# Optimization experiments

Hardware: AMD Instinct MI355X
Metric: run time of the kernel (lower is better)

Reference implementation:

```python
import jax, jax.numpy as jnp
import numpy as np

DIM = 1024
N_HEADS = 16
HEAD_DIM = DIM // N_HEADS
LN_EPS = 1e-5


def layer_norm(x, gamma, beta):
    mu = jnp.mean(x, axis=-1, keepdims=True)
    var = jnp.var(x, axis=-1, keepdims=True)
    return (x - mu) * jax.lax.rsqrt(var + LN_EPS) * gamma + beta


def setup_inputs() -> dict:
    key = jax.random.key(0)
    ks = jax.random.split(key, 12)
    B, Nq, Nc, D = 2, 2048, 2048, DIM
    s = 1.0 / np.sqrt(D)
    return {
        "query": jax.random.normal(ks[0], (B, Nq, D), jnp.float32),
        "context": jax.random.normal(ks[1], (B, Nc, D), jnp.float32),
        "Wq": jax.random.normal(ks[2], (D, D), jnp.float32) * s,
        "bq": jnp.zeros((D,), jnp.float32),
        "Wk": jax.random.normal(ks[3], (D, D), jnp.float32) * s,
        "bk": jnp.zeros((D,), jnp.float32),
        "Wv": jax.random.normal(ks[4], (D, D), jnp.float32) * s,
        "bv": jnp.zeros((D,), jnp.float32),
        "Wo": jax.random.normal(ks[5], (D, D), jnp.float32) * s,
        "bo": jnp.zeros((D,), jnp.float32),
        "gq": jnp.ones((D,), jnp.float32),
        "betaq": jnp.zeros((D,), jnp.float32),
        "gkv": jnp.ones((D,), jnp.float32),
        "betakv": jnp.zeros((D,), jnp.float32),
    }


def reference(query, context, Wq, bq, Wk, bk, Wv, bv, Wo, bo, gq, betaq, gkv, betakv):
    B, Nq, D = query.shape
    Nc = context.shape[1]
    residual = query
    q = layer_norm(query, gq, betaq)
    c = layer_norm(context, gkv, betakv)
    # projections; (B,N,D) -> (B,H,N,hd)
    Q = (q @ Wq + bq).reshape(B, Nq, N_HEADS, HEAD_DIM).transpose(0, 2, 1, 3)
    K = (c @ Wk + bk).reshape(B, Nc, N_HEADS, HEAD_DIM).transpose(0, 2, 1, 3)
    V = (c @ Wv + bv).reshape(B, Nc, N_HEADS, HEAD_DIM).transpose(0, 2, 1, 3)
    scores = jnp.einsum("bhqd,bhkd->bhqk", Q, K) / np.sqrt(HEAD_DIM).astype(np.float32)
    attn = jax.nn.softmax(scores, axis=-1)
    out = jnp.einsum("bhqk,bhkd->bhqd", attn, V)
    out = out.transpose(0, 2, 1, 3).reshape(B, Nq, D)
    return residual + out @ Wo + bo
```

## Files before the change

### kernel.cpp

```cpp
#include <hip/hip_runtime.h>
#include <hip/hip_bf16.h>

typedef unsigned short u16;
typedef unsigned long long u64;
typedef __bf16 bf16x8 __attribute__((ext_vector_type(8)));
typedef float f32x4 __attribute__((ext_vector_type(4)));

#define DIM 1024
#define NH 16
#define HD 64
#define QSCALE 0.180336880972788f

__device__ __forceinline__ u16 f2bf(float f) {
  union { float f; unsigned u; } v; v.f = f;
  unsigned r = v.u + 0x7fffu + ((v.u >> 16) & 1u);
  return (u16)(r >> 16);
}

__device__ __forceinline__ unsigned pk2(float a, float b) {
  union { __hip_bfloat162 h; unsigned u; } cv;
  cv.h = __float22bfloat162_rn(make_float2(a, b));
  return cv.u;
}

__device__ __forceinline__ float bf2f(unsigned s) {
  union { unsigned u; float f; } v; v.u = s << 16; return v.f;
}

__device__ __forceinline__ float fexp2(float x) {
#if __has_builtin(__builtin_amdgcn_exp2f)
  return __builtin_amdgcn_exp2f(x);
#else
  return exp2f(x);
#endif
}

__device__ __forceinline__ void gld16(const u16* gp, u16* lp) {
  __builtin_amdgcn_global_load_lds(
      (const __attribute__((address_space(1))) unsigned int*)(const void*)gp,
      (__attribute__((address_space(3))) unsigned int*)(void*)lp, 16, 0, 0);
}

__global__ __launch_bounds__(256) void prep_kernel(
    const float* __restrict__ q, const float* __restrict__ c,
    const float* __restrict__ gq, const float* __restrict__ bq,
    const float* __restrict__ gkv, const float* __restrict__ bkv,
    u16* __restrict__ qn, u16* __restrict__ cn,
    const float* W0, const float* W1, const float* W2, const float* W3,
    u16* O0, u16* O1, u16* O2, u16* O3) {
  __shared__ float red[2][4];
  __shared__ float t[32][33];
  int bid = blockIdx.x, tid = threadIdx.x;
  if (bid < 8192) {
    const float* x  = bid < 4096 ? q : c;
    const float* g  = bid < 4096 ? gq : gkv;
    const float* be = bid < 4096 ? bq : bkv;
    u16* out = bid < 4096 ? qn : cn;
    int row = bid & 4095;
    float4 v = ((const float4*)(x + (size_t)row * DIM))[tid];
    float s1 = v.x + v.y + v.z + v.w;
    float s2 = v.x * v.x + v.y * v.y + v.z * v.z + v.w * v.w;
#pragma unroll
    for (int o = 32; o >= 1; o >>= 1) { s1 += __shfl_xor(s1, o, 64); s2 += __shfl_xor(s2, o, 64); }
    int wv = tid >> 6;
    if ((tid & 63) == 0) { red[0][wv] = s1; red[1][wv] = s2; }
    __syncthreads();
    s1 = red[0][0] + red[0][1] + red[0][2] + red[0][3];
    s2 = red[1][0] + red[1][1] + red[1][2] + red[1][3];
    float mu = s1 * (1.f / DIM);
    float var = s2 * (1.f / DIM) - mu * mu;
    float rs = rsqrtf(var + 1e-5f);
    float4 gv = ((const float4*)g)[tid];
    float4 bv = ((const float4*)be)[tid];
    uint2 o2;
    o2.x = pk2((v.x - mu) * rs * gv.x + bv.x, (v.y - mu) * rs * gv.y + bv.y);
    o2.y = pk2((v.z - mu) * rs * gv.z + bv.z, (v.w - mu) * rs * gv.w + bv.w);
    ((uint2*)(out + (size_t)row * DIM))[tid] = o2;
  } else {
    int wid = bid - 8192;
    int z = wid >> 10;
    const float* W = z == 0 ? W0 : z == 1 ? W1 : z == 2 ? W2 : W3;
    u16* O        = z == 0 ? O0 : z == 1 ? O1 : z == 2 ? O2 : O3;
    int xy = wid & 1023;
    int bx = (xy & 31) * 32, by = (xy >> 5) * 32;
    int tx = tid & 31, ty = tid >> 5;
#pragma unroll
    for (int i = 0; i < 4; ++i) t[ty + i * 8][tx] = W[(size_t)(by + ty + i * 8) * DIM + bx + tx];
    __syncthreads();
#pragma unroll
    for (int i = 0; i < 4; ++i) O[(size_t)(bx + ty + i * 8) * DIM + by + tx] = f2bf(t[tx][ty + i * 8]);
  }
}

__global__ __launch_bounds__(256) void gemm_qkv(
    const u16* __restrict__ qn, const u16* __restrict__ cn,
    const u16* __restrict__ Wqt, const u16* __restrict__ Wkt, const u16* __restrict__ Wvt,
    const float* __restrict__ bq, const float* __restrict__ bk, const float* __restrict__ bv,
    u16* __restrict__ Qb, u16* __restrict__ Kb, u16* __restrict__ Vtb) {
  __shared__ __align__(16) u16 sm[(128 + 64 + 64) * 64];
  u16* As  = sm;
  u16* B0s = sm + 128 * 64;
  u16* B1s = sm + 192 * 64;
  int tid = threadIdx.x, wave = tid >> 6, lane = tid & 63;
  int lr = lane & 15, quad = lane >> 4;
  int m0 = blockIdx.x * 128, n0 = blockIdx.y * 64;
  int wm = (wave >> 1) * 64, wn = (wave & 1) * 32;

  if (blockIdx.z == 0) {
    f32x4 acck[4][2] = {}, accv[4][2] = {};
    for (int kt = 0; kt < DIM; kt += 64) {
#pragma unroll
      for (int r = 0; r < 4; ++r) {
        int slot = tid + r * 256;
        int row = slot >> 3;
        int c = (slot & 7) ^ (row & 7);
        gld16(cn + (size_t)(m0 + row) * DIM + kt + c * 8, &As[slot * 8]);
      }
      {
        int slot = tid;
        int row = slot >> 3;
        int c = (slot & 7) ^ (row & 7);
        gld16(Wkt + (size_t)(n0 + row) * DIM + kt + c * 8, &B0s[slot * 8]);
        gld16(Wvt + (size_t)(n0 + row) * DIM + kt + c * 8, &B1s[slot * 8]);
        slot = tid + 256; row = slot >> 3; c = (slot & 7) ^ (row & 7);
        gld16(Wkt + (size_t)(n0 + row) * DIM + kt + c * 8, &B0s[slot * 8]);
        gld16(Wvt + (size_t)(n0 + row) * DIM + kt + c * 8, &B1s[slot * 8]);
      }
      __syncthreads();
#pragma unroll
      for (int kc = 0; kc < 2; ++kc) {
        int pc = ((kc * 4 + quad) ^ (lr & 7)) * 8;
        bf16x8 af[4], b0f[2], b1f[2];
#pragma unroll
        for (int i = 0; i < 4; ++i) af[i] = *(const bf16x8*)&As[(wm + i * 16 + lr) * 64 + pc];
#pragma unroll
        for (int j = 0; j < 2; ++j) {
          b0f[j] = *(const bf16x8*)&B0s[(wn + j * 16 + lr) * 64 + pc];
          b1f[j] = *(const bf16x8*)&B1s[(wn + j * 16 + lr) * 64 + pc];
        }
#pragma unroll
        for (int mi = 0; mi < 4; ++mi)
#pragma unroll
          for (int ni = 0; ni < 2; ++ni) {
            acck[mi][ni] = __builtin_amdgcn_mfma_f32_16x16x32_bf16(af[mi], b0f[ni], acck[mi][ni], 0, 0, 0);
            accv[mi][ni] = __builtin_amdgcn_mfma_f32_16x16x32_bf16(b1f[ni], af[mi], accv[mi][ni], 0, 0, 0);
          }
      }
      __syncthreads();
    }
#pragma unroll
    for (int mi = 0; mi < 4; ++mi)
#pragma unroll
      for (int ni = 0; ni < 2; ++ni) {
        int col = n0 + wn + ni * 16 + lr;
        float bb_ = bk[col];
        int row0 = m0 + wm + mi * 16 + quad * 4;
#pragma unroll
        for (int r = 0; r < 4; ++r)
          Kb[(size_t)(row0 + r) * DIM + col] = f2bf(acck[mi][ni][r] + bb_);
      }
#pragma unroll
    for (int mi = 0; mi < 4; ++mi) {
      int m = m0 + wm + mi * 16 + lr;
      int bb = m >> 11, tt = m & 2047;
      u16* outb = Vtb + (((size_t)bb << 10)) * 2048 + tt;
#pragma unroll
      for (int ni = 0; ni < 2; ++ni) {
        int nbase = n0 + wn + ni * 16 + quad * 4;
#pragma unroll
        for (int r = 0; r < 4; ++r)
          outb[(size_t)(nbase + r) * 2048] = f2bf(accv[mi][ni][r] + bv[nbase + r]);
      }
    }
  } else {
    f32x4 acc[4][2] = {};
    for (int kt = 0; kt < DIM; kt += 64) {
#pragma unroll
      for (int r = 0; r < 4; ++r) {
        int slot = tid + r * 256;
        int row = slot >> 3;
        int c = (slot & 7) ^ (row & 7);
        gld16(qn + (size_t)(m0 + row) * DIM + kt + c * 8, &As[slot * 8]);
      }
#pragma unroll
      for (int r = 0; r < 2; ++r) {
        int slot = tid + r * 256;
        int row = slot >> 3;
        int c = (slot & 7) ^ (row & 7);
        gld16(Wqt + (size_t)(n0 + row) * DIM + kt + c * 8, &B0s[slot * 8]);
      }
      __syncthreads();
#pragma unroll
      for (int kc = 0; kc < 2; ++kc) {
        int pc = ((kc * 4 + quad) ^ (lr & 7)) * 8;
        bf16x8 af[4], b0f[2];
#pragma unroll
        for (int i = 0; i < 4; ++i) af[i] = *(const bf16x8*)&As[(wm + i * 16 + lr) * 64 + pc];
#pragma unroll
        for (int j = 0; j < 2; ++j) b0f[j] = *(const bf16x8*)&B0s[(wn + j * 16 + lr) * 64 + pc];
#pragma unroll
        for (int mi = 0; mi < 4; ++mi)
#pragma unroll
          for (int ni = 0; ni < 2; ++ni)
            acc[mi][ni] = __builtin_amdgcn_mfma_f32_16x16x32_bf16(af[mi], b0f[ni], acc[mi][ni], 0, 0, 0);
      }
      __syncthreads();
    }
#pragma unroll
    for (int mi = 0; mi < 4; ++mi)
#pragma unroll
      for (int ni = 0; ni < 2; ++ni) {
        int col = n0 + wn + ni * 16 + lr;
        float bb_ = bq[col];
        int row0 = m0 + wm + mi * 16 + quad * 4;
#pragma unroll
        for (int r = 0; r < 4; ++r)
          Qb[(size_t)(row0 + r) * DIM + col] = f2bf((acc[mi][ni][r] + bb_) * QSCALE);
      }
  }
}

__global__ __launch_bounds__(256) void gemm_o(const u16* __restrict__ A,
    const u16* __restrict__ Bt, const float* __restrict__ bias,
    float* __restrict__ out, const float* __restrict__ resid) {
  __shared__ __align__(16) u16 sm[(128 + 64) * 64];
  u16* As = sm;
  u16* Bs = sm + 128 * 64;
  int tid = threadIdx.x, wave = tid >> 6, lane = tid & 63;
  int lr = lane & 15, quad = lane >> 4;
  int m0 = blockIdx.x * 128, n0 = blockIdx.y * 64;
  int wm = (wave >> 1) * 64, wn = (wave & 1) * 32;
  f32x4 acc[4][2] = {};
  for (int kt = 0; kt < DIM; kt += 64) {
#pragma unroll
    for (int r = 0; r < 4; ++r) {
      int slot = tid + r * 256;
      int row = slot >> 3;
      int c = (slot & 7) ^ (row & 7);
      gld16(A + (size_t)(m0 + row) * DIM + kt + c * 8, &As[slot * 8]);
    }
#pragma unroll
    for (int r = 0; r < 2; ++r) {
      int slot = tid + r * 256;
      int row = slot >> 3;
      int c = (slot & 7) ^ (row & 7);
      gld16(Bt + (size_t)(n0 + row) * DIM + kt + c * 8, &Bs[slot * 8]);
    }
    __syncthreads();
#pragma unroll
    for (int kc = 0; kc < 2; ++kc) {
      int pc = ((kc * 4 + quad) ^ (lr & 7)) * 8;
      bf16x8 af[4], bfr[2];
#pragma unroll
      for (int i = 0; i < 4; ++i) af[i] = *(const bf16x8*)&As[(wm + i * 16 + lr) * 64 + pc];
#pragma unroll
      for (int j = 0; j < 2; ++j) bfr[j] = *(const bf16x8*)&Bs[(wn + j * 16 + lr) * 64 + pc];
#pragma unroll
      for (int mi = 0; mi < 4; ++mi)
#pragma unroll
        for (int ni = 0; ni < 2; ++ni)
          acc[mi][ni] = __builtin_amdgcn_mfma_f32_16x16x32_bf16(af[mi], bfr[ni], acc[mi][ni], 0, 0, 0);
    }
    __syncthreads();
  }
#pragma unroll
  for (int mi = 0; mi < 4; ++mi)
#pragma unroll
    for (int ni = 0; ni < 2; ++ni) {
      int col = n0 + wn + ni * 16 + lr;
      float bv = bias[col];
      int row0 = m0 + wm + mi * 16 + quad * 4;
#pragma unroll
      for (int r = 0; r < 4; ++r) {
        int row = row0 + r;
        out[(size_t)row * DIM + col] = acc[mi][ni][r] + bv + resid[(size_t)row * DIM + col];
      }
    }
}

__global__ __launch_bounds__(256) void flash_kernel(const u16* __restrict__ Q,
    const u16* __restrict__ Kg, const u16* __restrict__ Vt,
    u16* __restrict__ O0, u16* __restrict__ O1,
    float* __restrict__ L0, float* __restrict__ L1) {
  __shared__ __align__(16) u16 lds[24576];
  int tid = threadIdx.x, wave = tid >> 6, lane = tid & 63;
  int lr = lane & 15, quad = lane >> 4;
  int bh = blockIdx.x, b = bh >> 4, h = bh & 15;
  int q0 = blockIdx.y * 128;
  int split = blockIdx.z;
  u16* Op = split ? O1 : O0;
  float* Lp = split ? L1 : L0;
  int t0 = split * 1024;

  const u16* kbase = Kg + (size_t)(b * 2048 + t0) * DIM + h * HD;
  const u16* vbase = Vt + (size_t)(b * 1024 + h * HD) * 2048 + t0;

  bf16x8 qf[2][2];
#pragma unroll
  for (int s = 0; s < 2; ++s)
#pragma unroll
    for (int kc = 0; kc < 2; ++kc)
      qf[s][kc] = *(const bf16x8*)&Q[((size_t)(b * 2048 + q0 + wave * 32 + s * 16 + lr)) * DIM +
                                     h * HD + kc * 32 + quad * 8];

  int slot0 = tid, slot1 = tid + 256;
  int r0 = slot0 >> 3, c0 = (slot0 & 7) ^ (r0 & 7);
  int r1 = slot1 >> 3, c1 = (slot1 & 7) ^ (r1 & 7);
  const u16* kp0 = kbase + (size_t)r0 * DIM + c0 * 8;
  const u16* kp1 = kbase + (size_t)r1 * DIM + c1 * 8;
  const u16* vp0 = vbase + (size_t)r0 * 2048 + c0 * 8;
  const u16* vp1 = vbase + (size_t)r1 * 2048 + c1 * 8;

  gld16(kp0, &lds[slot0 * 8]);
  gld16(kp1, &lds[slot1 * 8]);
  gld16(vp0, &lds[8192 + slot0 * 8]);
  gld16(vp1, &lds[8192 + slot1 * 8]);
  __syncthreads();

  u16* Pw = &lds[16384 + wave * 2048];
  float plsum[2] = {0.f, 0.f};
  f32x4 oacc[2][4] = {};

  for (int j = 0; j < 16; ++j) {
    int par = j & 1;
    const u16* kcb = &lds[par * 4096];
    const u16* vcb = &lds[8192 + par * 4096];
    if (j < 15) {
      int np = par ^ 1;
      kp0 += 64 * DIM; kp1 += 64 * DIM; vp0 += 64; vp1 += 64;
      gld16(kp0, &lds[np * 4096 + slot0 * 8]);
      gld16(kp1, &lds[np * 4096 + slot1 * 8]);
      gld16(vp0, &lds[8192 + np * 4096 + slot0 * 8]);
      gld16(vp1, &lds[8192 + np * 4096 + slot1 * 8]);
    }

    f32x4 sf[2][4] = {};
#pragma unroll
    for (int kc = 0; kc < 2; ++kc) {
      int pc = ((kc * 4 + quad) ^ (lr & 7)) * 8;
#pragma unroll
      for (int ns = 0; ns < 4; ++ns) {
        bf16x8 kf = *(const bf16x8*)&kcb[(ns * 16 + lr) * 64 + pc];
#pragma unroll
        for (int s = 0; s < 2; ++s)
          sf[s][ns] = __builtin_amdgcn_mfma_f32_16x16x32_bf16(kf, qf[s][kc], sf[s][ns], 0, 0, 0);
      }
    }

#pragma unroll
    for (int s = 0; s < 2; ++s)
#pragma unroll
      for (int ns = 0; ns < 4; ++ns) {
        float p0 = fexp2(sf[s][ns][0]), p1 = fexp2(sf[s][ns][1]);
        float p2 = fexp2(sf[s][ns][2]), p3 = fexp2(sf[s][ns][3]);
        plsum[s] += (p0 + p1) + (p2 + p3);
        uint2 pk;
        pk.x = pk2(p0, p1);
        pk.y = pk2(p2, p3);
        int chunk = ns * 2 + (quad >> 1);
        int off = (s * 16 + lr) * 64 + ((chunk ^ (lr & 7)) * 8) + (quad & 1) * 4;
        *(uint2*)&Pw[off] = pk;
      }
    __threadfence_block();

#pragma unroll
    for (int kc = 0; kc < 2; ++kc) {
      int pc = ((kc * 4 + quad) ^ (lr & 7)) * 8;
      bf16x8 pf[2];
#pragma unroll
      for (int s = 0; s < 2; ++s)
        pf[s] = *(const bf16x8*)&Pw[(s * 16 + lr) * 64 + pc];
#pragma unroll
      for (int ds = 0; ds < 4; ++ds) {
        bf16x8 vf = *(const bf16x8*)&vcb[(ds * 16 + lr) * 64 + pc];
#pragma unroll
        for (int s = 0; s < 2; ++s)
          oacc[s][ds] = __builtin_amdgcn_mfma_f32_16x16x32_bf16(vf, pf[s], oacc[s][ds], 0, 0, 0);
      }
    }
    __syncthreads();
  }

#pragma unroll
  for (int s = 0; s < 2; ++s) {
    float l = plsum[s];
    l += __shfl_xor(l, 16, 64);
    l += __shfl_xor(l, 32, 64);
    size_t qrow = (size_t)(b * 2048 + q0 + wave * 32 + s * 16 + lr);
    if (quad == 0) Lp[qrow * 16 + h] = l;
#pragma unroll
    for (int ds = 0; ds < 4; ++ds) {
      uint2 pk;
      pk.x = pk2(oacc[s][ds][0], oacc[s][ds][1]);
      pk.y = pk2(oacc[s][ds][2], oacc[s][ds][3]);
      *(uint2*)&Op[qrow * DIM + h * HD + ds * 16 + quad * 4] = pk;
    }
  }
}

__global__ __launch_bounds__(256) void combine_kernel(const u16* __restrict__ O0,
    const u16* __restrict__ O1, const float* __restrict__ L0, const float* __restrict__ L1,
    u16* __restrict__ AO) {
  int row = blockIdx.x, tid = threadIdx.x;
  int h = tid >> 4;
  float rl = 1.f / (L0[row * 16 + h] + L1[row * 16 + h]);
  uint2 a = ((const uint2*)(O0 + (size_t)row * DIM))[tid];
  uint2 b = ((const uint2*)(O1 + (size_t)row * DIM))[tid];
  float v0 = (bf2f(a.x & 0xffff) + bf2f(b.x & 0xffff)) * rl;
  float v1 = (bf2f(a.x >> 16)    + bf2f(b.x >> 16))    * rl;
  float v2 = (bf2f(a.y & 0xffff) + bf2f(b.y & 0xffff)) * rl;
  float v3 = (bf2f(a.y >> 16)    + bf2f(b.y >> 16))    * rl;
  uint2 o;
  o.x = pk2(v0, v1);
  o.y = pk2(v2, v3);
  ((uint2*)(AO + (size_t)row * DIM))[tid] = o;
}

extern "C" void kernel_launch(void* const* d_in, const int* in_sizes, int n_in,
                              void* d_out, int out_size, void* d_ws, size_t ws_size,
                              hipStream_t stream) {
  const float* query   = (const float*)d_in[0];
  const float* context = (const float*)d_in[1];
  const float* Wq = (const float*)d_in[2];
  const float* bq = (const float*)d_in[3];
  const float* Wk = (const float*)d_in[4];
  const float* bk = (const float*)d_in[5];
  const float* Wv = (const float*)d_in[6];
  const float* bv = (const float*)d_in[7];
  const float* Wo = (const float*)d_in[8];
  const float* bo = (const float*)d_in[9];
  const float* gq    = (const float*)d_in[10];
  const float* betaq = (const float*)d_in[11];
  const float* gkv   = (const float*)d_in[12];
  const float* betakv= (const float*)d_in[13];
  (void)in_sizes; (void)n_in; (void)out_size; (void)ws_size;

  char* ws = (char*)d_ws;
  const size_t MB = (size_t)1 << 20;
  u16* qn  = (u16*)(ws + 0 * MB);
  u16* cn  = (u16*)(ws + 8 * MB);
  u16* Wqt = (u16*)(ws + 16 * MB);
  u16* Wkt = (u16*)(ws + 18 * MB);
  u16* Wvt = (u16*)(ws + 20 * MB);
  u16* Wot = (u16*)(ws + 22 * MB);
  u16* Qb  = (u16*)(ws + 24 * MB);
  u16* Kb  = (u16*)(ws + 32 * MB);
  u16* Vtb = (u16*)(ws + 40 * MB);
  u16* AOb = (u16*)(ws + 48 * MB);
  u16* Op0 = qn;
  u16* Op1 = cn;
  float* L0 = (float*)(ws + 16 * MB);
  float* L1 = (float*)(ws + 16 * MB + 256 * 1024);

  prep_kernel<<<12288, 256, 0, stream>>>(query, context, gq, betaq, gkv, betakv,
                                         qn, cn, Wq, Wk, Wv, Wo, Wqt, Wkt, Wvt, Wot);

  gemm_qkv<<<dim3(32, 16, 2), 256, 0, stream>>>(qn, cn, Wqt, Wkt, Wvt,
                                                bq, bk, bv, Qb, Kb, Vtb);

  flash_kernel<<<dim3(32, 16, 2), 256, 0, stream>>>(Qb, Kb, Vtb, Op0, Op1, L0, L1);

  combine_kernel<<<4096, 256, 0, stream>>>(Op0, Op1, L0, L1, AOb);

  gemm_o<<<dim3(32, 16), 256, 0, stream>>>(AOb, Wot, bo, (float*)d_out, query);
}
```

Measured before the change: 222.7 us.

## Switch flash attention to 32x32x16 MFMA with register-resident P via permlane32 swap

Rewrites the flash attention inner loop to use 32x32x16 bf16 MFMA tiles instead of 16x16x32. The exponentiated scores are packed and rearranged in registers with v_permlane32_swap, so they feed the PV matmul directly and no longer round-trip through the LDS P buffer with a block fence. This shrinks LDS usage, adds occupancy launch bounds and s_setprio hints around the MFMA sections. It risks register pressure from the larger accumulators, and correctness depends on the permlane layout matching the MFMA operand layout.

Measured after the change: 215.2 us. 3.4% less time.

```diff
diff --git a/kernel.cpp b/kernel.cpp
--- a/kernel.cpp
+++ b/kernel.cpp
@@ -5,6 +5,8 @@
 typedef unsigned long long u64;
 typedef __bf16 bf16x8 __attribute__((ext_vector_type(8)));
 typedef float f32x4 __attribute__((ext_vector_type(4)));
+typedef float f32x16 __attribute__((ext_vector_type(16)));
+typedef unsigned u32x4 __attribute__((ext_vector_type(4)));
 
 #define DIM 1024
 #define NH 16
@@ -39,6 +41,10 @@
   __builtin_amdgcn_global_load_lds(
       (const __attribute__((address_space(1))) unsigned int*)(const void*)gp,
       (__attribute__((address_space(3))) unsigned int*)(void*)lp, 16, 0, 0);
+}
+
+__device__ __forceinline__ void pl32swap(unsigned& a, unsigned& b) {
+  asm volatile("v_permlane32_swap_b32 %0, %1" : "+v"(a), "+v"(b));
 }
 
 __global__ __launch_bounds__(256) void prep_kernel(
@@ -278,13 +284,13 @@
     }
 }
 
-__global__ __launch_bounds__(256) void flash_kernel(const u16* __restrict__ Q,
+__global__ __launch_bounds__(256, 4) void flash_kernel(const u16* __restrict__ Q,
     const u16* __restrict__ Kg, const u16* __restrict__ Vt,
     u16* __restrict__ O0, u16* __restrict__ O1,
     float* __restrict__ L0, float* __restrict__ L1) {
-  __shared__ __align__(16) u16 lds[24576];
+  __shared__ __align__(16) u16 lds[16384];
   int tid = threadIdx.x, wave = tid >> 6, lane = tid & 63;
-  int lr = lane & 15, quad = lane >> 4;
+  int ln = lane & 31, hi = lane >> 5;
   int bh = blockIdx.x, b = bh >> 4, h = bh & 15;
   int q0 = blockIdx.y * 128;
   int split = blockIdx.z;
@@ -295,13 +301,11 @@
   const u16* kbase = Kg + (size_t)(b * 2048 + t0) * DIM + h * HD;
   const u16* vbase = Vt + (size_t)(b * 1024 + h * HD) * 2048 + t0;
 
-  bf16x8 qf[2][2];
-#pragma unroll
-  for (int s = 0; s < 2; ++s)
-#pragma unroll
-    for (int kc = 0; kc < 2; ++kc)
-      qf[s][kc] = *(const bf16x8*)&Q[((size_t)(b * 2048 + q0 + wave * 32 + s * 16 + lr)) * DIM +
-                                     h * HD + kc * 32 + quad * 8];
+  size_t qrow = (size_t)(b * 2048 + q0 + wave * 32 + ln);
+  bf16x8 qf[4];
+#pragma unroll
+  for (int ds = 0; ds < 4; ++ds)
+    qf[ds] = *(const bf16x8*)&Q[qrow * DIM + h * HD + ds * 16 + hi * 8];
 
   int slot0 = tid, slot1 = tid + 256;
   int r0 = slot0 >> 3, c0 = (slot0 & 7) ^ (r0 & 7);
@@ -317,9 +321,8 @@
   gld16(vp1, &lds[8192 + slot1 * 8]);
   __syncthreads();
 
-  u16* Pw = &lds[16384 + wave * 2048];
-  float plsum[2] = {0.f, 0.f};
-  f32x4 oacc[2][4] = {};
+  float plsum = 0.f;
+  f32x16 oacc[2] = {};
 
   for (int j = 0; j < 16; ++j) {
     int par = j & 1;
@@ -334,68 +337,64 @@
       gld16(vp1, &lds[8192 + np * 4096 + slot1 * 8]);
     }
 
-    f32x4 sf[2][4] = {};
-#pragma unroll
-    for (int kc = 0; kc < 2; ++kc) {
-      int pc = ((kc * 4 + quad) ^ (lr & 7)) * 8;
-#pragma unroll
-      for (int ns = 0; ns < 4; ++ns) {
-        bf16x8 kf = *(const bf16x8*)&kcb[(ns * 16 + lr) * 64 + pc];
-#pragma unroll
-        for (int s = 0; s < 2; ++s)
-          sf[s][ns] = __builtin_amdgcn_mfma_f32_16x16x32_bf16(kf, qf[s][kc], sf[s][ns], 0, 0, 0);
-      }
-    }
-
-#pragma unroll
-    for (int s = 0; s < 2; ++s)
-#pragma unroll
-      for (int ns = 0; ns < 4; ++ns) {
-        float p0 = fexp2(sf[s][ns][0]), p1 = fexp2(sf[s][ns][1]);
-        float p2 = fexp2(sf[s][ns][2]), p3 = fexp2(sf[s][ns][3]);
-        plsum[s] += (p0 + p1) + (p2 + p3);
-        uint2 pk;
-        pk.x = pk2(p0, p1);
-        pk.y = pk2(p2, p3);
-        int chunk = ns * 2 + (quad >> 1);
-        int off = (s * 16 + lr) * 64 + ((chunk ^ (lr & 7)) * 8) + (quad & 1) * 4;
-        *(uint2*)&Pw[off] = pk;
-      }
-    __threadfence_block();
-
-#pragma unroll
-    for (int kc = 0; kc < 2; ++kc) {
-      int pc = ((kc * 4 + quad) ^ (lr & 7)) * 8;
-      bf16x8 pf[2];
-#pragma unroll
-      for (int s = 0; s < 2; ++s)
-        pf[s] = *(const bf16x8*)&Pw[(s * 16 + lr) * 64 + pc];
+    f32x16 sf[2] = {};
+    __builtin_amdgcn_s_setprio(1);
+#pragma unroll
+    for (int kt2 = 0; kt2 < 2; ++kt2) {
+      int rs = (kt2 * 32 + ln) * 64;
+      int rx = (kt2 * 32 + ln) & 7;
 #pragma unroll
       for (int ds = 0; ds < 4; ++ds) {
-        bf16x8 vf = *(const bf16x8*)&vcb[(ds * 16 + lr) * 64 + pc];
-#pragma unroll
-        for (int s = 0; s < 2; ++s)
-          oacc[s][ds] = __builtin_amdgcn_mfma_f32_16x16x32_bf16(vf, pf[s], oacc[s][ds], 0, 0, 0);
-      }
-    }
+        bf16x8 kf = *(const bf16x8*)&kcb[rs + (((ds * 2 + hi) ^ rx) * 8)];
+        sf[kt2] = __builtin_amdgcn_mfma_f32_32x32x16_bf16(kf, qf[ds], sf[kt2], 0, 0, 0);
+      }
+    }
+    __builtin_amdgcn_s_setprio(0);
+
+    bf16x8 pb[4];
+#pragma unroll
+    for (int kt2 = 0; kt2 < 2; ++kt2)
+#pragma unroll
+      for (int ks = 0; ks < 2; ++ks) {
+        float e0 = fexp2(sf[kt2][ks * 8 + 0]), e1 = fexp2(sf[kt2][ks * 8 + 1]);
+        float e2 = fexp2(sf[kt2][ks * 8 + 2]), e3 = fexp2(sf[kt2][ks * 8 + 3]);
+        float e4 = fexp2(sf[kt2][ks * 8 + 4]), e5 = fexp2(sf[kt2][ks * 8 + 5]);
+        float e6 = fexp2(sf[kt2][ks * 8 + 6]), e7 = fexp2(sf[kt2][ks * 8 + 7]);
+        plsum += ((e0 + e1) + (e2 + e3)) + ((e4 + e5) + (e6 + e7));
+        unsigned w0 = pk2(e0, e1), w1 = pk2(e2, e3);
+        unsigned w2 = pk2(e4, e5), w3 = pk2(e6, e7);
+        pl32swap(w0, w2);
+        pl32swap(w1, w3);
+        u32x4 t; t.x = w0; t.y = w1; t.z = w2; t.w = w3;
+        pb[kt2 * 2 + ks] = __builtin_bit_cast(bf16x8, t);
+      }
+
+    __builtin_amdgcn_s_setprio(1);
+#pragma unroll
+    for (int dt = 0; dt < 2; ++dt) {
+      int rs = (dt * 32 + ln) * 64;
+      int rx = (dt * 32 + ln) & 7;
+#pragma unroll
+      for (int kk = 0; kk < 4; ++kk) {
+        bf16x8 vf = *(const bf16x8*)&vcb[rs + (((kk * 2 + hi) ^ rx) * 8)];
+        oacc[dt] = __builtin_amdgcn_mfma_f32_32x32x16_bf16(vf, pb[kk], oacc[dt], 0, 0, 0);
+      }
+    }
+    __builtin_amdgcn_s_setprio(0);
     __syncthreads();
   }
 
-#pragma unroll
-  for (int s = 0; s < 2; ++s) {
-    float l = plsum[s];
-    l += __shfl_xor(l, 16, 64);
-    l += __shfl_xor(l, 32, 64);
-    size_t qrow = (size_t)(b * 2048 + q0 + wave * 32 + s * 16 + lr);
-    if (quad == 0) Lp[qrow * 16 + h] = l;
-#pragma unroll
-    for (int ds = 0; ds < 4; ++ds) {
+  float l = plsum + __shfl_xor(plsum, 32, 64);
+  if (hi == 0) Lp[qrow * 16 + h] = l;
+#pragma unroll
+  for (int dt = 0; dt < 2; ++dt)
+#pragma unroll
+    for (int g = 0; g < 4; ++g) {
       uint2 pk;
-      pk.x = pk2(oacc[s][ds][0], oacc[s][ds][1]);
-      pk.y = pk2(oacc[s][ds][2], oacc[s][ds][3]);
-      *(uint2*)&Op[qrow * DIM + h * HD + ds * 16 + quad * 4] = pk;
-    }
-  }
+      pk.x = pk2(oacc[dt][g * 4 + 0], oacc[dt][g * 4 + 1]);
+      pk.y = pk2(oacc[dt][g * 4 + 2], oacc[dt][g * 4 + 3]);
+      *(uint2*)&Op[qrow * DIM + h * HD + dt * 32 + g * 8 + hi * 4] = pk;
+    }
 }
 
 __global__ __launch_bounds__(256) void combine_kernel(const u16* __restrict__ O0,
```
